# Performance work log

Measured on AMD Instinct MI355X. Metric: run time of the kernel, lower is better.

The kernel has to match this reference:

```python
import jax, jax.numpy as jnp
import numpy as np
import math

B, D, OUT, K = 128, 128, 100000, 4096
T = 0.07
# NOTE: original code reads momentum as params[4], which is -1 (params = [K, T, -1, -1, -1, momentum]).
# We replicate this faithfully: effective momentum = -1.0.
MOMENTUM = -1.0


def setup_inputs() -> dict:
    key = jax.random.key(0)
    k1, k2, k3, k4, k5, k6, k7 = jax.random.split(key, 7)
    stdv = 1.0 / math.sqrt(D / 3)
    return {
        "z1": jax.random.normal(k1, (B, D), dtype=jnp.float32),
        "z2": jax.random.normal(k2, (B, D), dtype=jnp.float32),
        "z3": jax.random.normal(k3, (B, D), dtype=jnp.float32),
        "memory_z2": jax.random.uniform(k4, (OUT, D), dtype=jnp.float32, minval=-stdv, maxval=stdv),
        "memory_z3": jax.random.uniform(k5, (OUT, D), dtype=jnp.float32, minval=-stdv, maxval=stdv),
        "y": jax.random.randint(k6, (B,), 0, OUT, dtype=jnp.int32),
        "idx": jax.random.randint(k7, (B, K + 1), 0, OUT, dtype=jnp.int32),
    }


def _scores(memory, idx, z1, outputSize):
    # gather [B, K+1, D] rows, per-row dot with z1 -> [B, K+1]
    w = jax.lax.stop_gradient(memory)[idx]
    s = jnp.exp(jnp.einsum('bkd,bd->bk', w, z1) / T)[..., None]  # [B, K+1, 1]
    Z = jax.lax.stop_gradient(jnp.mean(s) * outputSize)  # Z_* set on first call
    return s / Z


def _update(memory, y, z):
    pos = memory[y] * MOMENTUM + z * (1.0 - MOMENTUM)  # [B, D]
    pos = pos / jnp.sqrt(jnp.sum(pos * pos, axis=1, keepdims=True))
    return memory.at[y].set(pos)


def reference(z1, z2, z3, memory_z2, memory_z3, y, idx):
    outputSize = memory_z2.shape[0]
    # mimic idx=None path: first column of idx is the positive index y
    idx = idx.at[:, 0].set(y)
    I_z12 = _scores(memory_z2, idx, z1, outputSize)
    I_z13 = _scores(memory_z3, idx, z1, outputSize)
    new_mem2 = _update(memory_z2, y, z2)
    new_mem3 = _update(memory_z3, y, z3)
    return (I_z12, I_z13, new_mem2, new_mem3)
```

## Files before the change

### kernel.cpp

```cpp
#include <hip/hip_runtime.h>

#define BB   128
#define DD   128
#define OUTN 100000
#define KP1  4097
#define TEMP 0.07f

#define NSB   8320
#define NPB   2080
#define ITERS 4
#define N1F4  3200000
#define NF4   6400000
#define SCORES (2 * BB * KP1)
#define NSCALE_BLK 4097

typedef float vfloat4 __attribute__((ext_vector_type(4)));

__global__ __launch_bounds__(256) void fused_kernel(
    const float* __restrict__ z1,
    const float* __restrict__ mem2,
    const float* __restrict__ mem3,
    const int*   __restrict__ y,
    const int*   __restrict__ idx,
    float* __restrict__ out,
    float* __restrict__ part)
{
    const int bid = blockIdx.x;
    const int tid = threadIdx.x;
    const int g   = tid & 7;
    const int grp = tid >> 3;

    int jj0[ITERS], jj1[ITERS];
    #pragma unroll
    for (int it = 0; it < ITERS; ++it) {
        const int sb    = bid + it * NPB;
        const int b     = sb & (BB - 1);
        const int chunk = sb >> 7;
        const int k0    = chunk * 64 + grp;
        const int k1    = k0 + 32;
        int j0 = 0, j1 = 0;
        if (k0 < KP1) j0 = (k0 == 0) ? y[b] : idx[b * KP1 + k0];
        if (k1 < KP1) j1 = idx[b * KP1 + k1];
        jj0[it] = j0;  jj1[it] = j1;
    }

    float acc2 = 0.f, acc3 = 0.f;

    #pragma unroll
    for (int it = 0; it < ITERS; ++it) {
        const int sb    = bid + it * NPB;
        const int b     = sb & (BB - 1);
        const int chunk = sb >> 7;

        const float4* zz = (const float4*)(z1 + (size_t)b * DD + g * 16);
        const float4 z0 = zz[0], zv1 = zz[1], zv2 = zz[2], zv3 = zz[3];

        #pragma unroll
        for (int p = 0; p < 2; ++p) {
            const int k     = chunk * 64 + p * 32 + grp;
            const bool valid = (k < KP1);
            const int j     = p ? jj1[it] : jj0[it];

            const float4* r2 = (const float4*)(mem2 + (size_t)j * DD + g * 16);
            const float4* r3 = (const float4*)(mem3 + (size_t)j * DD + g * 16);
            const float4 a0 = r2[0], a1 = r2[1], a2 = r2[2], a3 = r2[3];
            const float4 c0 = r3[0], c1 = r3[1], c2 = r3[2], c3 = r3[3];

            float d2 = a0.x*z0.x  + a0.y*z0.y  + a0.z*z0.z  + a0.w*z0.w
                     + a1.x*zv1.x + a1.y*zv1.y + a1.z*zv1.z + a1.w*zv1.w
                     + a2.x*zv2.x + a2.y*zv2.y + a2.z*zv2.z + a2.w*zv2.w
                     + a3.x*zv3.x + a3.y*zv3.y + a3.z*zv3.z + a3.w*zv3.w;
            float d3 = c0.x*z0.x  + c0.y*z0.y  + c0.z*z0.z  + c0.w*z0.w
                     + c1.x*zv1.x + c1.y*zv1.y + c1.z*zv1.z + c1.w*zv1.w
                     + c2.x*zv2.x + c2.y*zv2.y + c2.z*zv2.z + c2.w*zv2.w
                     + c3.x*zv3.x + c3.y*zv3.y + c3.z*zv3.z + c3.w*zv3.w;

            d2 += __shfl_xor(d2, 1);  d3 += __shfl_xor(d3, 1);
            d2 += __shfl_xor(d2, 2);  d3 += __shfl_xor(d3, 2);
            d2 += __shfl_xor(d2, 4);  d3 += __shfl_xor(d3, 4);

            if (valid && g == 0) {
                const float s2 = expf(d2 * (1.0f / TEMP));
                const float s3 = expf(d3 * (1.0f / TEMP));
                out[b * KP1 + k]            = s2;
                out[BB * KP1 + b * KP1 + k] = s3;
                acc2 += s2;
                acc3 += s3;
            }
        }
    }

    {
        const vfloat4* m2f = (const vfloat4*)mem2;
        const vfloat4* m3f = (const vfloat4*)mem3;
        vfloat4* dstf = (vfloat4*)(out + SCORES);
        for (int i = bid * 256 + tid; i < NF4; i += NPB * 256) {
            const vfloat4 v = (i < N1F4) ? m2f[i] : m3f[i - N1F4];
            __builtin_nontemporal_store(v, dstf + i);
        }
    }

    acc2 += __shfl_xor(acc2, 8);   acc3 += __shfl_xor(acc3, 8);
    acc2 += __shfl_xor(acc2, 16);  acc3 += __shfl_xor(acc3, 16);
    acc2 += __shfl_xor(acc2, 32);  acc3 += __shfl_xor(acc3, 32);

    __shared__ float w2s[4], w3s[4];
    const int wave = tid >> 6;
    const int lane = tid & 63;
    if (lane == 0) { w2s[wave] = acc2; w3s[wave] = acc3; }
    __syncthreads();
    if (tid == 0) {
        const float t2 = w2s[0] + w2s[1] + w2s[2] + w2s[3];
        const float t3 = w3s[0] + w3s[1] + w3s[2] + w3s[3];
        const int slot = bid & 63;
        atomicAdd(&part[slot],      t2);
        atomicAdd(&part[64 + slot], t3);
    }
}

__global__ __launch_bounds__(256) void finalize_kernel(
    const float* __restrict__ z2,
    const float* __restrict__ z3,
    const float* __restrict__ mem2,
    const float* __restrict__ mem3,
    const int*   __restrict__ y,
    float* __restrict__ out,
    const float* __restrict__ part)
{
    const int t = threadIdx.x;

    if (blockIdx.x < NSCALE_BLK) {
        __shared__ float sc[2];
        if (t == 0) {
            float t2 = 0.f, t3 = 0.f;
            for (int i = 0; i < 64; ++i) { t2 += part[i]; t3 += part[64 + i]; }
            sc[0] = (float)((double)(BB * KP1) / ((double)OUTN * (double)t2));
            sc[1] = (float)((double)(BB * KP1) / ((double)OUTN * (double)t3));
        }
        __syncthreads();
        const int i = blockIdx.x * 256 + t;
        out[i] *= sc[(i < BB * KP1) ? 0 : 1];
        return;
    }

    const int b  = blockIdx.x - NSCALE_BLK;
    const int yb = y[b];

    __shared__ int dup;
    if (t == 0) dup = 0;
    __syncthreads();
    if (t > b && t < BB && y[t] == yb) dup = 1;
    __syncthreads();
    if (dup) return;
    if (t >= 64) return;

    float* out2 = out + SCORES;
    float* out3 = out2 + OUTN * DD;

    const float2 m2 = *(const float2*)(mem2 + (size_t)yb * DD + 2 * t);
    const float2 m3 = *(const float2*)(mem3 + (size_t)yb * DD + 2 * t);
    const float2 a2 = *(const float2*)(z2 + b * DD + 2 * t);
    const float2 a3 = *(const float2*)(z3 + b * DD + 2 * t);

    float2 p2, p3;
    p2.x = 2.f * a2.x - m2.x;  p2.y = 2.f * a2.y - m2.y;
    p3.x = 2.f * a3.x - m3.x;  p3.y = 2.f * a3.y - m3.y;

    float ss2 = p2.x * p2.x + p2.y * p2.y;
    float ss3 = p3.x * p3.x + p3.y * p3.y;
    #pragma unroll
    for (int off = 32; off > 0; off >>= 1) {
        ss2 += __shfl_xor(ss2, off);
        ss3 += __shfl_xor(ss3, off);
    }
    const float inv2 = 1.f / sqrtf(ss2);
    const float inv3 = 1.f / sqrtf(ss3);

    float2 w2, w3;
    w2.x = p2.x * inv2;  w2.y = p2.y * inv2;
    w3.x = p3.x * inv3;  w3.y = p3.y * inv3;
    *(float2*)(out2 + (size_t)yb * DD + 2 * t) = w2;
    *(float2*)(out3 + (size_t)yb * DD + 2 * t) = w3;
}

extern "C" void kernel_launch(void* const* d_in, const int* in_sizes, int n_in,
                              void* d_out, int out_size, void* d_ws, size_t ws_size,
                              hipStream_t stream)
{
    const float* z1   = (const float*)d_in[0];
    const float* z2   = (const float*)d_in[1];
    const float* z3   = (const float*)d_in[2];
    const float* mem2 = (const float*)d_in[3];
    const float* mem3 = (const float*)d_in[4];
    const int*   y    = (const int*)d_in[5];
    const int*   idx  = (const int*)d_in[6];
    float*       out  = (float*)d_out;
    float*       part = (float*)d_ws;

    hipMemsetAsync(d_ws, 0, 128 * sizeof(float), stream);

    fused_kernel<<<NPB, 256, 0, stream>>>(z1, mem2, mem3, y, idx, out, part);

    finalize_kernel<<<NSCALE_BLK + BB, 256, 0, stream>>>(
        z2, z3, mem2, mem3, y, out, part);
}
```

Before: 275.7 us.

## Replace per-sample row gather with dense tiled GEMM over memory and bucketed score scatter

Instead of gathering each sampled memory row per (batch, k) pair, the kernel now computes scores against every memory row in tiles of 128 rows using an LDS-tiled fp32 GEMM over all 128 batch vectors. It reuses the same tile loads to do the required memory copy to the output. A preceding kernel buckets the sampled (b, k) indices by memory tile via atomics and transposes z1, so each GEMM block scatters exp-scores only for the requested pairs. This trades the heavily redundant random gather traffic for about 6.5 GFLOP of dense compute plus extra atomics. Bucket capacity is fixed, so heavily skewed indices could overflow and drop entries.

New measurement: 499.2 us. 81.1% more time.

```diff
diff --git a/kernel.cpp b/kernel.cpp
--- a/kernel.cpp
+++ b/kernel.cpp
@@ -6,115 +6,171 @@
 #define KP1  4097
 #define TEMP 0.07f
 
-#define NSB   8320
-#define NPB   2080
-#define ITERS 4
-#define N1F4  3200000
-#define NF4   6400000
+#define TJ   128
+#define NT   782
+#define CAP  1536
 #define SCORES (2 * BB * KP1)
+#define NROW (OUTN * DD)
 #define NSCALE_BLK 4097
 
+#define WS_CNT_OFF 128
+#define WS_Z1T_OFF 1024
+#define WS_BKT_OFF 17408
+
 typedef float vfloat4 __attribute__((ext_vector_type(4)));
 
-__global__ __launch_bounds__(256) void fused_kernel(
-    const float* __restrict__ z1,
-    const float* __restrict__ mem2,
-    const float* __restrict__ mem3,
-    const int*   __restrict__ y,
-    const int*   __restrict__ idx,
-    float* __restrict__ out,
-    float* __restrict__ part)
-{
-    const int bid = blockIdx.x;
-    const int tid = threadIdx.x;
-    const int g   = tid & 7;
-    const int grp = tid >> 3;
-
-    int jj0[ITERS], jj1[ITERS];
+__global__ __launch_bounds__(256) void count_prep_kernel(
+    const float* __restrict__ z1, const int* __restrict__ y,
+    const int* __restrict__ idx, float* __restrict__ ws)
+{
+    const int b = blockIdx.y;
+    if (blockIdx.x == 17) {
+        float* z1t = ws + WS_Z1T_OFF;
+        const int t = threadIdx.x;
+        if (t < DD) z1t[t * BB + b] = z1[b * DD + t];
+        return;
+    }
+    int* cnt = (int*)(ws + WS_CNT_OFF);
+    unsigned* bkt = (unsigned*)(ws + WS_BKT_OFF);
+    const int k = blockIdx.x * 256 + threadIdx.x;
+    if (k >= KP1) return;
+    const int j = (k == 0) ? y[b] : idx[b * KP1 + k];
+    const int tile = j >> 7, jl = j & 127;
+    const int pos = atomicAdd(&cnt[tile], 1);
+    if (pos < CAP)
+        bkt[tile * CAP + pos] =
+            ((unsigned)jl << 20) | ((unsigned)b << 13) | (unsigned)k;
+}
+
+__global__ __launch_bounds__(256) void gemm_kernel(
+    const float* __restrict__ mem2, const float* __restrict__ mem3,
+    float* __restrict__ ws, float* __restrict__ out)
+{
+    __shared__ float lds[8192];
+    vfloat4* abuf = (vfloat4*)lds;
+    vfloat4* zbuf = ((vfloat4*)lds) + 1024;
+    const int t  = threadIdx.x;
+    const int tx = t & 15;
+    const int ty = t >> 4;
+    const int tile = blockIdx.x;
+    const long jt = (long)tile * TJ;
+
+    const float* z1t = ws + WS_Z1T_OFF;
+    const int*   cnt = (const int*)(ws + WS_CNT_OFF);
+    const unsigned* bkt = (const unsigned*)(ws + WS_BKT_OFF);
+    const int ncnt = min(cnt[tile], CAP);
+    const vfloat4* zf = (const vfloat4*)z1t;
+
+    float zacc2 = 0.f, zacc3 = 0.f;
+
+    for (int m = 0; m < 2; ++m) {
+        const vfloat4* mem = (const vfloat4*)(m ? mem3 : mem2);
+        vfloat4* cd = (vfloat4*)(out + SCORES + (size_t)m * NROW);
+        float* so = out + (size_t)m * BB * KP1;
+
+        float acc[8][8];
+        #pragma unroll
+        for (int a = 0; a < 8; ++a)
+            #pragma unroll
+            for (int q = 0; q < 8; ++q) acc[a][q] = 0.f;
+
+        for (int c = 0; c < 4; ++c) {
+            __syncthreads();
+
+            vfloat4 av[4]; int asl[4];
+            #pragma unroll
+            for (int i = 0; i < 4; ++i) {
+                const int e = i * 256 + t;
+                const int j = e >> 3, c4 = e & 7;
+                const long gj = jt + j;
+                vfloat4 v = {0.f, 0.f, 0.f, 0.f};
+                if (gj < OUTN) {
+                    v = mem[gj * 32 + c * 8 + c4];
+                    __builtin_nontemporal_store(v, cd + gj * 32 + c * 8 + c4);
+                }
+                av[i] = v;
+                asl[i] = j * 8 + ((c4 ^ (j >> 3)) & 7);
+            }
+            #pragma unroll
+            for (int i = 0; i < 4; ++i) {
+                const int e = i * 256 + t;
+                const int dd = e >> 5, bq = e & 31;
+                zbuf[e] = zf[(c * 32 + dd) * 32 + bq];
+            }
+            #pragma unroll
+            for (int i = 0; i < 4; ++i) abuf[asl[i]] = av[i];
+            __syncthreads();
+
+            #pragma unroll
+            for (int d4 = 0; d4 < 8; ++d4) {
+                vfloat4 zA[4], zB[4];
+                #pragma unroll
+                for (int q = 0; q < 4; ++q) {
+                    zA[q] = zbuf[(d4 * 4 + q) * 32 + tx];
+                    zB[q] = zbuf[(d4 * 4 + q) * 32 + 16 + tx];
+                }
+                #pragma unroll
+                for (int h = 0; h < 2; ++h) {
+                    vfloat4 mj[4];
+                    #pragma unroll
+                    for (int r = 0; r < 4; ++r)
+                        mj[r] = abuf[(ty * 8 + h * 4 + r) * 8 + ((d4 ^ ty) & 7)];
+                    #pragma unroll
+                    for (int q = 0; q < 4; ++q)
+                        #pragma unroll
+                        for (int r = 0; r < 4; ++r) {
+                            const float mv = mj[r][q];
+                            #pragma unroll
+                            for (int i = 0; i < 4; ++i) {
+                                acc[h * 4 + r][i]     += mv * zA[q][i];
+                                acc[h * 4 + r][4 + i] += mv * zB[q][i];
+                            }
+                        }
+                }
+            }
+        }
+
+        #pragma unroll
+        for (int h2 = 0; h2 < 2; ++h2) {
+            __syncthreads();
+            if ((ty >> 3) == h2) {
+                vfloat4* Sh = (vfloat4*)lds;
+                #pragma unroll
+                for (int jj = 0; jj < 8; ++jj) {
+                    const int jl2 = (ty & 7) * 8 + jj;
+                    vfloat4 o0 = {acc[jj][0], acc[jj][1], acc[jj][2], acc[jj][3]};
+                    vfloat4 o1 = {acc[jj][4], acc[jj][5], acc[jj][6], acc[jj][7]};
+                    Sh[jl2 * 32 + tx]      = o0;
+                    Sh[jl2 * 32 + 16 + tx] = o1;
+                }
+            }
+            __syncthreads();
+            for (int e = t; e < ncnt; e += 256) {
+                const unsigned p = bkt[tile * CAP + e];
+                const int jl = (int)(p >> 20);
+                if ((jl >> 6) != h2) continue;
+                const int eb = (int)((p >> 13) & 127);
+                const int ek = (int)(p & 0x1FFF);
+                const float s = expf(lds[(jl & 63) * 128 + eb] * (1.0f / TEMP));
+                so[eb * KP1 + ek] = s;
+                if (m) zacc3 += s; else zacc2 += s;
+            }
+        }
+    }
+
     #pragma unroll
-    for (int it = 0; it < ITERS; ++it) {
-        const int sb    = bid + it * NPB;
-        const int b     = sb & (BB - 1);
-        const int chunk = sb >> 7;
-        const int k0    = chunk * 64 + grp;
-        const int k1    = k0 + 32;
-        int j0 = 0, j1 = 0;
-        if (k0 < KP1) j0 = (k0 == 0) ? y[b] : idx[b * KP1 + k0];
-        if (k1 < KP1) j1 = idx[b * KP1 + k1];
-        jj0[it] = j0;  jj1[it] = j1;
-    }
-
-    float acc2 = 0.f, acc3 = 0.f;
-
-    #pragma unroll
-    for (int it = 0; it < ITERS; ++it) {
-        const int sb    = bid + it * NPB;
-        const int b     = sb & (BB - 1);
-        const int chunk = sb >> 7;
-
-        const float4* zz = (const float4*)(z1 + (size_t)b * DD + g * 16);
-        const float4 z0 = zz[0], zv1 = zz[1], zv2 = zz[2], zv3 = zz[3];
-
-        #pragma unroll
-        for (int p = 0; p < 2; ++p) {
-            const int k     = chunk * 64 + p * 32 + grp;
-            const bool valid = (k < KP1);
-            const int j     = p ? jj1[it] : jj0[it];
-
-            const float4* r2 = (const float4*)(mem2 + (size_t)j * DD + g * 16);
-            const float4* r3 = (const float4*)(mem3 + (size_t)j * DD + g * 16);
-            const float4 a0 = r2[0], a1 = r2[1], a2 = r2[2], a3 = r2[3];
-            const float4 c0 = r3[0], c1 = r3[1], c2 = r3[2], c3 = r3[3];
-
-            float d2 = a0.x*z0.x  + a0.y*z0.y  + a0.z*z0.z  + a0.w*z0.w
-                     + a1.x*zv1.x + a1.y*zv1.y + a1.z*zv1.z + a1.w*zv1.w
-                     + a2.x*zv2.x + a2.y*zv2.y + a2.z*zv2.z + a2.w*zv2.w
-                     + a3.x*zv3.x + a3.y*zv3.y + a3.z*zv3.z + a3.w*zv3.w;
-            float d3 = c0.x*z0.x  + c0.y*z0.y  + c0.z*z0.z  + c0.w*z0.w
-                     + c1.x*zv1.x + c1.y*zv1.y + c1.z*zv1.z + c1.w*zv1.w
-                     + c2.x*zv2.x + c2.y*zv2.y + c2.z*zv2.z + c2.w*zv2.w
-                     + c3.x*zv3.x + c3.y*zv3.y + c3.z*zv3.z + c3.w*zv3.w;
-
-            d2 += __shfl_xor(d2, 1);  d3 += __shfl_xor(d3, 1);
-            d2 += __shfl_xor(d2, 2);  d3 += __shfl_xor(d3, 2);
-            d2 += __shfl_xor(d2, 4);  d3 += __shfl_xor(d3, 4);
-
-            if (valid && g == 0) {
-                const float s2 = expf(d2 * (1.0f / TEMP));
-                const float s3 = expf(d3 * (1.0f / TEMP));
-                out[b * KP1 + k]            = s2;
-                out[BB * KP1 + b * KP1 + k] = s3;
-                acc2 += s2;
-                acc3 += s3;
-            }
-        }
-    }
-
-    {
-        const vfloat4* m2f = (const vfloat4*)mem2;
-        const vfloat4* m3f = (const vfloat4*)mem3;
-        vfloat4* dstf = (vfloat4*)(out + SCORES);
-        for (int i = bid * 256 + tid; i < NF4; i += NPB * 256) {
-            const vfloat4 v = (i < N1F4) ? m2f[i] : m3f[i - N1F4];
-            __builtin_nontemporal_store(v, dstf + i);
-        }
-    }
-
-    acc2 += __shfl_xor(acc2, 8);   acc3 += __shfl_xor(acc3, 8);
-    acc2 += __shfl_xor(acc2, 16);  acc3 += __shfl_xor(acc3, 16);
-    acc2 += __shfl_xor(acc2, 32);  acc3 += __shfl_xor(acc3, 32);
-
+    for (int off = 32; off > 0; off >>= 1) {
+        zacc2 += __shfl_xor(zacc2, off);
+        zacc3 += __shfl_xor(zacc3, off);
+    }
     __shared__ float w2s[4], w3s[4];
-    const int wave = tid >> 6;
-    const int lane = tid & 63;
-    if (lane == 0) { w2s[wave] = acc2; w3s[wave] = acc3; }
+    const int wave = t >> 6, lane = t & 63;
+    if (lane == 0) { w2s[wave] = zacc2; w3s[wave] = zacc3; }
     __syncthreads();
-    if (tid == 0) {
-        const float t2 = w2s[0] + w2s[1] + w2s[2] + w2s[3];
-        const float t3 = w3s[0] + w3s[1] + w3s[2] + w3s[3];
-        const int slot = bid & 63;
-        atomicAdd(&part[slot],      t2);
-        atomicAdd(&part[64 + slot], t3);
+    if (t == 0) {
+        const int slot = tile & 63;
+        atomicAdd(&ws[slot],      w2s[0] + w2s[1] + w2s[2] + w2s[3]);
+        atomicAdd(&ws[64 + slot], w3s[0] + w3s[1] + w3s[2] + w3s[3]);
     }
 }
 
@@ -155,7 +211,7 @@
     if (t >= 64) return;
 
     float* out2 = out + SCORES;
-    float* out3 = out2 + OUTN * DD;
+    float* out3 = out2 + NROW;
 
     const float2 m2 = *(const float2*)(mem2 + (size_t)yb * DD + 2 * t);
     const float2 m3 = *(const float2*)(mem3 + (size_t)yb * DD + 2 * t);
@@ -195,12 +251,15 @@
     const int*   y    = (const int*)d_in[5];
     const int*   idx  = (const int*)d_in[6];
     float*       out  = (float*)d_out;
-    float*       part = (float*)d_ws;
-
-    hipMemsetAsync(d_ws, 0, 128 * sizeof(float), stream);
-
-    fused_kernel<<<NPB, 256, 0, stream>>>(z1, mem2, mem3, y, idx, out, part);
+    float*       ws   = (float*)d_ws;
+
+    hipMemsetAsync(d_ws, 0, 4096, stream);
+
+    dim3 gc(18, BB);
+    count_prep_kernel<<<gc, 256, 0, stream>>>(z1, y, idx, ws);
+
+    gemm_kernel<<<NT, 256, 0, stream>>>(mem2, mem3, ws, out);
 
     finalize_kernel<<<NSCALE_BLK + BB, 256, 0, stream>>>(
-        z2, z3, mem2, mem3, y, out, part);
-}
+        z2, z3, mem2, mem3, y, out, ws);
+}
```
